# Kernel tuning notes

Measured on AMD Instinct MI355X. Metric: run time of the kernel, lower is better.

Reference implementation:

```python
import jax, jax.numpy as jnp
import numpy as np

HEADS = 16
D_HEAD = 64
EPS = 1e-5


def _ln(x, g, b):
    m = jnp.mean(x, axis=-1, keepdims=True)
    v = jnp.var(x, axis=-1, keepdims=True)
    return (x - m) * jax.lax.rsqrt(v + EPS) * g + b


def _attn(xq, xc, Wq, Wk, Wv, Wo, bo):
    # Wq: [dim, inner], Wk/Wv: [ctx_dim, inner], Wo: [inner, dim]
    B, N, _ = xq.shape
    S = xc.shape[1]
    q = (xq @ Wq).reshape(B, N, HEADS, D_HEAD)
    k = (xc @ Wk).reshape(B, S, HEADS, D_HEAD)
    v = (xc @ Wv).reshape(B, S, HEADS, D_HEAD)
    scale = D_HEAD ** -0.5
    scores = jnp.einsum('bnhd,bshd->bhns', q, k) * scale
    attn = jax.nn.softmax(scores, axis=-1)
    out = jnp.einsum('bhns,bshd->bnhd', attn, v).reshape(B, N, HEADS * D_HEAD)
    return out @ Wo + bo


def _geglu_ff(x, Wp, bp, Wf, bf):
    h = x @ Wp + bp  # [B,N,2*inner]
    a, gate = jnp.split(h, 2, axis=-1)
    # torch F.gelu default is exact (erf) gelu
    return (a * jax.nn.gelu(gate, approximate=False)) @ Wf + bf


def setup_inputs() -> dict:
    key = jax.random.key(0)
    ks = jax.random.split(key, 16)
    dim, ctx, inner, ffin = 1024, 768, HEADS * D_HEAD, 4 * 1024
    def w(k, i, o):
        return jax.random.normal(k, (i, o), jnp.float32) * (i ** -0.5)
    inp = {
        'x': jax.random.normal(ks[0], (4, 2048, dim), jnp.float32),
        'context': jax.random.normal(ks[1], (4, 77, ctx), jnp.float32),
        'Wq1': w(ks[2], dim, inner), 'Wk1': w(ks[3], dim, inner), 'Wv1': w(ks[4], dim, inner),
        'Wo1': w(ks[5], inner, dim), 'bo1': jnp.zeros((dim,), jnp.float32),
        'Wq2': w(ks[6], dim, inner), 'Wk2': w(ks[7], ctx, inner), 'Wv2': w(ks[8], ctx, inner),
        'Wo2': w(ks[9], inner, dim), 'bo2': jnp.zeros((dim,), jnp.float32),
        'Wp': w(ks[10], dim, 2 * ffin), 'bp': jnp.zeros((2 * ffin,), jnp.float32),
        'Wf': w(ks[11], ffin, dim), 'bf': jnp.zeros((dim,), jnp.float32),
        'g1': jnp.ones((dim,), jnp.float32), 'b1': jnp.zeros((dim,), jnp.float32),
        'g2': jnp.ones((dim,), jnp.float32), 'b2': jnp.zeros((dim,), jnp.float32),
        'g3': jnp.ones((dim,), jnp.float32), 'b3': jnp.zeros((dim,), jnp.float32),
    }
    return inp


def reference(x, context, Wq1, Wk1, Wv1, Wo1, bo1, Wq2, Wk2, Wv2, Wo2, bo2,
              Wp, bp, Wf, bf, g1, b1, g2, b2, g3, b3):
    x = _attn(_ln(x, g1, b1), _ln(x, g1, b1), Wq1, Wk1, Wv1, Wo1, bo1) + x
    x = _attn(_ln(x, g2, b2), context, Wq2, Wk2, Wv2, Wo2, bo2) + x
    x = _geglu_ff(_ln(x, g3, b3), Wp, bp, Wf, bf) + x
    return x
```

## Files before the change

### kernel.cpp

```cpp
#include <hip/hip_runtime.h>

typedef unsigned short u16;
typedef __bf16 bf16x8 __attribute__((ext_vector_type(8)));
typedef float f32x4 __attribute__((ext_vector_type(4)));

#define HEADS 16
#define DHEAD 64
#define DIM 1024
#define NTOK 2048
#define BATCH 4
#define CTXD 768
#define SCROSS 77
#define FFIN 4096

__device__ inline float bf2f(u16 v) { return __uint_as_float(((unsigned)v) << 16); }
__device__ inline u16 f2bf(float f) {
    unsigned u = __float_as_uint(f);
    unsigned r = u + 0x7fffu + ((u >> 16) & 1u);
    return (u16)(r >> 16);
}
__device__ inline f32x4 f4zero() { f32x4 v; v[0]=0.f; v[1]=0.f; v[2]=0.f; v[3]=0.f; return v; }
__device__ inline bf16x8 as_bf16x8(uint4 u) { union { uint4 a; bf16x8 b; } c; c.a = u; return c.b; }

__device__ inline void gload_lds16(const u16* g, u16* l) {
    __builtin_amdgcn_global_load_lds((const __attribute__((address_space(1))) unsigned*)g,
                                     (__attribute__((address_space(3))) unsigned*)l, 16, 0, 0);
}

__global__ __launch_bounds__(256) void wt_k(const float* __restrict__ W, u16* __restrict__ WT,
                                            int K, int N, float scale, int remap) {
    __shared__ u16 Ts[64][72];
    int k0 = blockIdx.x * 64, n0 = blockIdx.y * 64;
    int t = threadIdx.x;
    int r = t >> 2, c4 = (t & 3) * 16;
    const float* wp = W + (size_t)(k0 + r) * N + n0 + c4;
    #pragma unroll
    for (int j = 0; j < 4; j++) {
        float4 v = *(const float4*)(wp + j * 4);
        Ts[c4 + j * 4 + 0][r] = f2bf(v.x * scale);
        Ts[c4 + j * 4 + 1][r] = f2bf(v.y * scale);
        Ts[c4 + j * 4 + 2][r] = f2bf(v.z * scale);
        Ts[c4 + j * 4 + 3][r] = f2bf(v.w * scale);
    }
    __syncthreads();
    int n = t >> 2, kc = (t & 3) * 16;
    int ng = n0 + n;
    if (remap) ng = ((ng & 4095) >> 4) * 32 + ((ng >> 12) << 4) + (ng & 15);
    u16* op = WT + (size_t)ng * K + k0 + kc;
    *(uint4*)op       = *(const uint4*)&Ts[n][kc];
    *(uint4*)(op + 8) = *(const uint4*)&Ts[n][kc + 8];
}

__global__ __launch_bounds__(256) void cvt_k(const float* __restrict__ X, u16* __restrict__ Y, int n4) {
    int i = blockIdx.x * 256 + threadIdx.x;
    if (i < n4) {
        float4 v = *(const float4*)(X + (size_t)i * 4);
        uint2 o;
        o.x = (unsigned)f2bf(v.x) | ((unsigned)f2bf(v.y) << 16);
        o.y = (unsigned)f2bf(v.z) | ((unsigned)f2bf(v.w) << 16);
        *(uint2*)(Y + (size_t)i * 4) = o;
    }
}

__global__ __launch_bounds__(256) void ln_k(const float* __restrict__ X, const float* __restrict__ G,
                                            const float* __restrict__ Bt, u16* __restrict__ Y) {
    int row = blockIdx.x;
    int t = threadIdx.x;
    int w = t >> 6, lane = t & 63;
    float4 xv = *(const float4*)(X + (size_t)row * DIM + t * 4);
    float s = xv.x + xv.y + xv.z + xv.w;
    float s2 = xv.x*xv.x + xv.y*xv.y + xv.z*xv.z + xv.w*xv.w;
    for (int off = 1; off < 64; off <<= 1) {
        s  += __shfl_xor(s,  off, 64);
        s2 += __shfl_xor(s2, off, 64);
    }
    __shared__ float rs[4], rs2[4];
    if (lane == 0) { rs[w] = s; rs2[w] = s2; }
    __syncthreads();
    float S_ = rs[0] + rs[1] + rs[2] + rs[3];
    float S2_ = rs2[0] + rs2[1] + rs2[2] + rs2[3];
    float mean = S_ * (1.0f / DIM);
    float var = fmaxf(S2_ * (1.0f / DIM) - mean * mean, 0.f);
    float rstd = rsqrtf(var + 1e-5f);
    int col = t * 4;
    float4 g = *(const float4*)(G + col);
    float4 b = *(const float4*)(Bt + col);
    float y0 = (xv.x - mean) * rstd * g.x + b.x;
    float y1 = (xv.y - mean) * rstd * g.y + b.y;
    float y2 = (xv.z - mean) * rstd * g.z + b.z;
    float y3 = (xv.w - mean) * rstd * g.w + b.w;
    uint2 o;
    o.x = (unsigned)f2bf(y0) | ((unsigned)f2bf(y1) << 16);
    o.y = (unsigned)f2bf(y2) | ((unsigned)f2bf(y3) << 16);
    *(uint2*)(Y + (size_t)row * DIM + col) = o;
}

template<typename TC, bool RESID>
__global__ __launch_bounds__(256) void gemm128(const u16* __restrict__ A, int lda,
                                               const u16* __restrict__ BT,
                                               const float* __restrict__ bias, const float* resid,
                                               TC* C, int ldc, int M, int N, int K) {
    __shared__ __align__(16) u16 As[128 * 32];
    __shared__ __align__(16) u16 Bs[128 * 32];
    int m0 = blockIdx.x * 128, n0 = blockIdx.y * 128;
    int t = threadIdx.x;
    int w = t >> 6, lane = t & 63;
    int quad = lane >> 4, l16 = lane & 15;
    int mh = (w & 1) * 64, nh = (w >> 1) * 64;
    f32x4 acc[4][4];
    #pragma unroll
    for (int i = 0; i < 4; i++)
        #pragma unroll
        for (int j = 0; j < 4; j++) acc[i][j] = f4zero();
    int sr = t >> 2;
    int sc8 = (t & 3) * 8;
    int ra0 = min(m0 + sr, M - 1);
    int ra1 = min(m0 + sr + 64, M - 1);
    const u16* ga0 = A + (size_t)ra0 * lda + sc8;
    const u16* ga1 = A + (size_t)ra1 * lda + sc8;
    const u16* gb0 = BT + (size_t)(n0 + sr) * K + sc8;
    const u16* gb1 = BT + (size_t)(n0 + sr + 64) * K + sc8;
    u16* lA0 = &As[w * 512];
    u16* lA1 = &As[2048 + w * 512];
    u16* lB0 = &Bs[w * 512];
    u16* lB1 = &Bs[2048 + w * 512];
    for (int k0 = 0; k0 < K; k0 += 32) {
        __syncthreads();
        gload_lds16(ga0 + k0, lA0);
        gload_lds16(ga1 + k0, lA1);
        gload_lds16(gb0 + k0, lB0);
        gload_lds16(gb1 + k0, lB1);
        __syncthreads();
        bf16x8 af[4], bfv[4];
        #pragma unroll
        for (int i = 0; i < 4; i++) {
            af[i]  = as_bf16x8(*(const uint4*)&As[(mh + i * 16 + l16) * 32 + quad * 8]);
            bfv[i] = as_bf16x8(*(const uint4*)&Bs[(nh + i * 16 + l16) * 32 + quad * 8]);
        }
        #pragma unroll
        for (int i = 0; i < 4; i++)
            #pragma unroll
            for (int j = 0; j < 4; j++)
                acc[i][j] = __builtin_amdgcn_mfma_f32_16x16x32_bf16(af[i], bfv[j], acc[i][j], 0, 0, 0);
    }
    #pragma unroll
    for (int j = 0; j < 4; j++) {
        int gn = n0 + nh + j * 16 + l16;
        float bv = bias ? bias[gn] : 0.f;
        #pragma unroll
        for (int i = 0; i < 4; i++) {
            #pragma unroll
            for (int r = 0; r < 4; r++) {
                int gm = m0 + mh + i * 16 + quad * 4 + r;
                if (gm < M) {
                    float v = acc[i][j][r] + bv;
                    if constexpr (RESID) v += resid[(size_t)gm * N + gn];
                    if constexpr (__is_same(TC, u16)) C[(size_t)gm * ldc + gn] = f2bf(v);
                    else                              C[(size_t)gm * ldc + gn] = v;
                }
            }
        }
    }
}


#define BAR() __builtin_amdgcn_s_barrier()
#define SB0() __builtin_amdgcn_sched_barrier(0)
#define PRIO1() __builtin_amdgcn_s_setprio(1)
#define PRIO0() __builtin_amdgcn_s_setprio(0)
#define WAIT_VM6() asm volatile("s_waitcnt vmcnt(6)" ::: "memory")
#define WAIT_VM0() asm volatile("s_waitcnt vmcnt(0)" ::: "memory")
#define WAIT_LGKM0() asm volatile("s_waitcnt lgkmcnt(0)" ::: "memory")
#define WAIT_LGKM8() asm volatile("s_waitcnt lgkmcnt(8)" ::: "memory")

#define STAGE_A_R(P, h, q, TAU) gload_lds16(gA + (size_t)((h) * 128 + (q) * 64) * 1024 + (TAU) * 64, \
                                            lA + (P) * 16384 + (h) * 8192 + (q) * 4096)
#define STAGE_B_R(P, h, q, TAU) gload_lds16(gB + (size_t)((h) * 128 + (q) * 64) * 1024 + (TAU) * 64, \
                                            lB + (P) * 16384 + (h) * 8192 + (q) * 4096)
#define RD_A(P, fi, ks) as_bf16x8(*(const uint4*)(rdA + (P) * 32768 + (fi) * 2048 + ((ks) ? o1 : o0)))
#define RD_B(P, fj, ks) as_bf16x8(*(const uint4*)(rdB + (P) * 32768 + (fj) * 2048 + ((ks) ? o1 : o0)))
#define MM(ai, aj, av, bv) acc[ai][aj] = __builtin_amdgcn_mfma_f32_16x16x32_bf16(av, bv, acc[ai][aj], 0, 0, 0)

#define TILE256(P, S0, S1, T, LAST) do {                                              \
    if (LAST) { WAIT_VM0(); } else { WAIT_VM6(); }                                    \
    BAR(); SB0();                                                                     \
                               \
    Ar[0][0] = RD_A(P, 0, 0); Ar[0][1] = RD_A(P, 0, 1);                               \
    Ar[1][0] = RD_A(P, 1, 0); Ar[1][1] = RD_A(P, 1, 1);                               \
    Ar[2][0] = RD_A(P, 2, 0); Ar[2][1] = RD_A(P, 2, 1);                               \
    Ar[3][0] = RD_A(P, 3, 0); Ar[3][1] = RD_A(P, 3, 1);                               \
    Br[0][0] = RD_B(P, 0, 0); Br[0][1] = RD_B(P, 0, 1);                               \
    Br[1][0] = RD_B(P, 1, 0); Br[1][1] = RD_B(P, 1, 1);                               \
    if (S0) { STAGE_B_R((P) ^ 1, 1, 0, (T) + 1); STAGE_B_R((P) ^ 1, 1, 1, (T) + 1); } \
    WAIT_LGKM8();                                                                     \
    BAR(); WAIT_LGKM0(); SB0(); PRIO1();                                              \
    MM(0,0,Ar[0][0],Br[0][0]); MM(1,0,Ar[1][0],Br[0][0]); MM(2,0,Ar[2][0],Br[0][0]); MM(3,0,Ar[3][0],Br[0][0]); \
    MM(0,1,Ar[0][0],Br[1][0]); MM(1,1,Ar[1][0],Br[1][0]); MM(2,1,Ar[2][0],Br[1][0]); MM(3,1,Ar[3][0],Br[1][0]); \
    MM(0,0,Ar[0][1],Br[0][1]); MM(1,0,Ar[1][1],Br[0][1]); MM(2,0,Ar[2][1],Br[0][1]); MM(3,0,Ar[3][1],Br[0][1]); \
    MM(0,1,Ar[0][1],Br[1][1]); MM(1,1,Ar[1][1],Br[1][1]); MM(2,1,Ar[2][1],Br[1][1]); MM(3,1,Ar[3][1],Br[1][1]); \
    PRIO0(); SB0(); BAR();                                                            \
                                                   \
    Br[0][0] = RD_B(P, 2, 0); Br[0][1] = RD_B(P, 2, 1);                               \
    Br[1][0] = RD_B(P, 3, 0); Br[1][1] = RD_B(P, 3, 1);                               \
    if (S1) { STAGE_A_R(P, 0, 0, (T) + 2); STAGE_A_R(P, 1, 0, (T) + 2); }             \
    BAR(); WAIT_LGKM0(); SB0(); PRIO1();                                              \
    MM(0,2,Ar[0][0],Br[0][0]); MM(1,2,Ar[1][0],Br[0][0]); MM(2,2,Ar[2][0],Br[0][0]); MM(3,2,Ar[3][0],Br[0][0]); \
    MM(0,3,Ar[0][0],Br[1][0]); MM(1,3,Ar[1][0],Br[1][0]); MM(2,3,Ar[2][0],Br[1][0]); MM(3,3,Ar[3][0],Br[1][0]); \
    MM(0,2,Ar[0][1],Br[0][1]); MM(1,2,Ar[1][1],Br[0][1]); MM(2,2,Ar[2][1],Br[0][1]); MM(3,2,Ar[3][1],Br[0][1]); \
    MM(0,3,Ar[0][1],Br[1][1]); MM(1,3,Ar[1][1],Br[1][1]); MM(2,3,Ar[2][1],Br[1][1]); MM(3,3,Ar[3][1],Br[1][1]); \
    PRIO0(); SB0(); BAR();                                                            \
                                                  \
    Ar[0][0] = RD_A(P, 4, 0); Ar[0][1] = RD_A(P, 4, 1);                               \
    Ar[1][0] = RD_A(P, 5, 0); Ar[1][1] = RD_A(P, 5, 1);                               \
    Ar[2][0] = RD_A(P, 6, 0); Ar[2][1] = RD_A(P, 6, 1);                               \
    Ar[3][0] = RD_A(P, 7, 0); Ar[3][1] = RD_A(P, 7, 1);                               \
    if (S1) { STAGE_A_R(P, 0, 1, (T) + 2); STAGE_A_R(P, 1, 1, (T) + 2); }             \
    BAR(); WAIT_LGKM0(); SB0(); PRIO1();                                              \
    MM(4,2,Ar[0][0],Br[0][0]); MM(5,2,Ar[1][0],Br[0][0]); MM(6,2,Ar[2][0],Br[0][0]); MM(7,2,Ar[3][0],Br[0][0]); \
    MM(4,3,Ar[0][0],Br[1][0]); MM(5,3,Ar[1][0],Br[1][0]); MM(6,3,Ar[2][0],Br[1][0]); MM(7,3,Ar[3][0],Br[1][0]); \
    MM(4,2,Ar[0][1],Br[0][1]); MM(5,2,Ar[1][1],Br[0][1]); MM(6,2,Ar[2][1],Br[0][1]); MM(7,2,Ar[3][1],Br[0][1]); \
    MM(4,3,Ar[0][1],Br[1][1]); MM(5,3,Ar[1][1],Br[1][1]); MM(6,3,Ar[2][1],Br[1][1]); MM(7,3,Ar[3][1],Br[1][1]); \
    PRIO0(); SB0(); BAR();                                                            \
                                              \
    Br[0][0] = RD_B(P, 0, 0); Br[0][1] = RD_B(P, 0, 1);                               \
    Br[1][0] = RD_B(P, 1, 0); Br[1][1] = RD_B(P, 1, 1);                               \
    if (S1) { STAGE_B_R(P, 0, 0, (T) + 2); STAGE_B_R(P, 0, 1, (T) + 2); }             \
    BAR(); WAIT_LGKM0(); SB0(); PRIO1();                                              \
    MM(4,0,Ar[0][0],Br[0][0]); MM(5,0,Ar[1][0],Br[0][0]); MM(6,0,Ar[2][0],Br[0][0]); MM(7,0,Ar[3][0],Br[0][0]); \
    MM(4,1,Ar[0][0],Br[1][0]); MM(5,1,Ar[1][0],Br[1][0]); MM(6,1,Ar[2][0],Br[1][0]); MM(7,1,Ar[3][0],Br[1][0]); \
    MM(4,0,Ar[0][1],Br[0][1]); MM(5,0,Ar[1][1],Br[0][1]); MM(6,0,Ar[2][1],Br[0][1]); MM(7,0,Ar[3][1],Br[0][1]); \
    MM(4,1,Ar[0][1],Br[1][1]); MM(5,1,Ar[1][1],Br[1][1]); MM(6,1,Ar[2][1],Br[1][1]); MM(7,1,Ar[3][1],Br[1][1]); \
    PRIO0(); SB0();                                                                   \
} while (0)

template<int NBY, int LDC, int EPI>
__global__ __launch_bounds__(512, 2) void gemm256(const u16* __restrict__ A,
                                                  const u16* __restrict__ BT,
                                                  const float* __restrict__ bias,
                                                  u16* __restrict__ C) {
    __shared__ __align__(16) u16 As[2][16384];
    __shared__ __align__(16) u16 Bs[2][16384];
    int t = threadIdx.x;
    int w = t >> 6, lane = t & 63;
    int quad = lane >> 4, l16 = lane & 15;
    int wm = w >> 2, wn = w & 3;
    int bid = blockIdx.x;
    int cpx = (int)gridDim.x >> 3;
    int swz = (bid & 7) * cpx + (bid >> 3);
    int bx = swz / NBY, by = swz % NBY;
    int m0 = bx << 8, n0 = by << 8;

    int ar = t >> 3;
    int ac = (((t & 7) ^ (ar & 7)) << 3);
    const u16* gA = A + (size_t)(m0 + ar) * 1024 + ac;
    const u16* gB = BT + (size_t)(n0 + ar) * 1024 + ac;
    u16* lA = &As[0][0] + (w << 9);
    u16* lB = &Bs[0][0] + (w << 9);
    const char* rdA = (const char*)&As[0][0] + (((wm << 7) + l16) << 7);
    const char* rdB = (const char*)&Bs[0][0] + (((wn << 6) + l16) << 7);
    int o0 = (quad << 4) ^ ((l16 & 7) << 4);
    int o1 = o0 ^ 64;

    f32x4 acc[8][4];
    #pragma unroll
    for (int i = 0; i < 8; i++)
        #pragma unroll
        for (int j = 0; j < 4; j++) acc[i][j] = f4zero();

    STAGE_A_R(0, 0, 0, 0); STAGE_A_R(0, 0, 1, 0); STAGE_A_R(0, 1, 0, 0); STAGE_A_R(0, 1, 1, 0);
    STAGE_B_R(0, 0, 0, 0); STAGE_B_R(0, 0, 1, 0); STAGE_B_R(0, 1, 0, 0); STAGE_B_R(0, 1, 1, 0);
    STAGE_A_R(1, 0, 0, 1); STAGE_A_R(1, 0, 1, 1); STAGE_A_R(1, 1, 0, 1); STAGE_A_R(1, 1, 1, 1);
    STAGE_B_R(1, 0, 0, 1); STAGE_B_R(1, 0, 1, 1);

    bf16x8 Ar[4][2], Br[2][2];
    #pragma unroll 1
    for (int tt = 0; tt < 14; tt += 2) {
        TILE256(0, 1, 1, tt, 0);
        TILE256(1, 1, 1, tt + 1, 0);
    }
    TILE256(0, 1, 0, 14, 0);
    TILE256(1, 0, 0, 15, 1);

    if constexpr (EPI == 0) {
        int gm0 = m0 + wm * 128 + quad * 4;
        int gn0 = n0 + wn * 64 + l16;
        #pragma unroll
        for (int fi = 0; fi < 8; fi++)
            #pragma unroll
            for (int fj = 0; fj < 4; fj++)
                #pragma unroll
                for (int r = 0; r < 4; r++)
                    C[(size_t)(gm0 + fi * 16 + r) * LDC + gn0 + fj * 16] = f2bf(acc[fi][fj][r]);
    } else {
        int gm0 = m0 + wm * 128 + quad * 4;
        int oc0 = (n0 >> 1) + wn * 32 + l16;
        #pragma unroll
        for (int jp = 0; jp < 2; jp++) {
            int oc = oc0 + jp * 16;
            float ba = bias[oc];
            float bg = bias[FFIN + oc];
            #pragma unroll
            for (int fi = 0; fi < 8; fi++)
                #pragma unroll
                for (int r = 0; r < 4; r++) {
                    float a = acc[fi][2 * jp][r] + ba;
                    float g = acc[fi][2 * jp + 1][r] + bg;
                    float v = a * (0.5f * g * (1.f + erff(g * 0.70710678118654752f)));
                    C[(size_t)(gm0 + fi * 16 + r) * LDC + oc] = f2bf(v);
                }
        }
    }
}

__global__ __launch_bounds__(256) void attn_k(const u16* Q, int ldq, const u16* __restrict__ K,
                                              const u16* __restrict__ V, int ldkv,
                                              u16* O, int S) {
    __shared__ __align__(16) u16 Ksh[2][4096];
    __shared__ __align__(16) u16 Vt[4][2048];
    __shared__ __align__(16) u16 Pb[4][4][512];
    int bh = blockIdx.x;
    int b = bh >> 4, h = bh & 15;
    int q0 = blockIdx.y * 64;
    int t = threadIdx.x;
    int w = t >> 6, lane = t & 63;
    int quad = lane >> 4, l16 = lane & 15;
    const u16* Qp = Q + ((size_t)b * NTOK + q0) * ldq + h * DHEAD;
    const u16* Kp = K + (size_t)b * S * ldkv + h * DHEAD;
    const u16* Vp = V + (size_t)b * S * ldkv + h * DHEAD;
    bf16x8 qf[2];
    #pragma unroll
    for (int ds = 0; ds < 2; ds++)
        qf[ds] = as_bf16x8(*(const uint4*)(Qp + (size_t)(w * 16 + l16) * ldq + ds * 32 + quad * 8));
    float l_l = 0.f;
    f32x4 o_acc[4];
    #pragma unroll
    for (int dt = 0; dt < 4; dt++) o_acc[dt] = f4zero();
    int cA = w * 128 + lane;
    int krA = cA >> 2, kdA = (cA & 3) * 8;
    int krB = (cA + 64) >> 2, kdB = ((cA + 64) & 3) * 8;
    int vd = (t >> 5) * 8;
    int vk = (t & 31) * 4;
    int vkk = vk >> 5, vcol = vk & 31;
    int nkt = (S + 127) / 128;
    for (int kt = 0; kt < nkt; kt++) {
        int kbase = kt * 128;
        bool full = (kbase + 128) <= S;
        __syncthreads();
        {
            int rA = min(kbase + krA, S - 1);
            int rB = min(kbase + krB, S - 1);
            const u16* kgA = Kp + (size_t)rA * ldkv;
            const u16* kgB = Kp + (size_t)rB * ldkv;
            gload_lds16(kgA + kdA,      &Ksh[0][w * 1024]);
            gload_lds16(kgB + kdB,      &Ksh[0][w * 1024 + 512]);
            gload_lds16(kgA + 32 + kdA, &Ksh[1][w * 1024]);
            gload_lds16(kgB + 32 + kdB, &Ksh[1][w * 1024 + 512]);
        }
        {
            union { uint4 u; u16 e[8]; } vr[4];
            #pragma unroll
            for (int j = 0; j < 4; j++) {
                int key = min(kbase + vk + j, S - 1);
                vr[j].u = *(const uint4*)(Vp + (size_t)key * ldkv + vd);
            }
            #pragma unroll
            for (int d = 0; d < 8; d++) {
                uint2 p;
                p.x = (unsigned)vr[0].e[d] | ((unsigned)vr[1].e[d] << 16);
                p.y = (unsigned)vr[2].e[d] | ((unsigned)vr[3].e[d] << 16);
                *(uint2*)&Vt[vkk][(vd + d) * 32 + vcol] = p;
            }
        }
        __syncthreads();
        f32x4 sc[8];
        #pragma unroll
        for (int sub = 0; sub < 8; sub++) {
            bf16x8 kf0 = as_bf16x8(*(const uint4*)&Ksh[0][(sub * 16 + l16) * 32 + quad * 8]);
            bf16x8 kf1 = as_bf16x8(*(const uint4*)&Ksh[1][(sub * 16 + l16) * 32 + quad * 8]);
            f32x4 s = __builtin_amdgcn_mfma_f32_16x16x32_bf16(kf0, qf[0], f4zero(), 0, 0, 0);
            sc[sub] = __builtin_amdgcn_mfma_f32_16x16x32_bf16(kf1, qf[1], s, 0, 0, 0);
        }
        if (!full) {
            #pragma unroll
            for (int sub = 0; sub < 8; sub++)
                #pragma unroll
                for (int r = 0; r < 4; r++)
                    if (kbase + sub * 16 + quad * 4 + r >= S) sc[sub][r] = -1e30f;
        }
        float psum = 0.f;
        #pragma unroll
        for (int sub = 0; sub < 8; sub++) {
            float p0 = __builtin_amdgcn_exp2f(sc[sub][0]);
            float p1 = __builtin_amdgcn_exp2f(sc[sub][1]);
            float p2 = __builtin_amdgcn_exp2f(sc[sub][2]);
            float p3 = __builtin_amdgcn_exp2f(sc[sub][3]);
            psum += (p0 + p1) + (p2 + p3);
            uint2 pk;
            pk.x = __builtin_amdgcn_perm(__float_as_uint(p1), __float_as_uint(p0), 0x07060302);
            pk.y = __builtin_amdgcn_perm(__float_as_uint(p3), __float_as_uint(p2), 0x07060302);
            *(uint2*)&Pb[w][sub >> 1][l16 * 32 + (sub & 1) * 16 + quad * 4] = pk;
        }
        l_l += psum;
        #pragma unroll
        for (int kk = 0; kk < 4; kk++) {
            bf16x8 pf = as_bf16x8(*(const uint4*)&Pb[w][kk][l16 * 32 + quad * 8]);
            #pragma unroll
            for (int dt = 0; dt < 4; dt++) {
                bf16x8 vf = as_bf16x8(*(const uint4*)&Vt[kk][(dt * 16 + l16) * 32 + quad * 8]);
                o_acc[dt] = __builtin_amdgcn_mfma_f32_16x16x32_bf16(pf, vf, o_acc[dt], 0, 0, 0);
            }
        }
    }
    float l_tot = l_l;
    l_tot += __shfl_xor(l_tot, 16, 64);
    l_tot += __shfl_xor(l_tot, 32, 64);
    #pragma unroll
    for (int r = 0; r < 4; r++) {
        float lr = __shfl(l_tot, quad * 4 + r, 64);
        float invl = (lr > 0.f) ? (1.f / lr) : 0.f;
        int gq = q0 + w * 16 + quad * 4 + r;
        #pragma unroll
        for (int dt = 0; dt < 4; dt++) {
            O[((size_t)b * NTOK + gq) * ldq + h * DHEAD + dt * 16 + l16] = f2bf(o_acc[dt][r] * invl);
        }
    }
}

extern "C" void kernel_launch(void* const* d_in, const int* in_sizes, int n_in,
                              void* d_out, int out_size, void* d_ws, size_t ws_size,
                              hipStream_t stream) {
    const float* x   = (const float*)d_in[0];
    const float* ctx = (const float*)d_in[1];
    const float* Wq1 = (const float*)d_in[2];
    const float* Wk1 = (const float*)d_in[3];
    const float* Wv1 = (const float*)d_in[4];
    const float* Wo1 = (const float*)d_in[5];
    const float* bo1 = (const float*)d_in[6];
    const float* Wq2 = (const float*)d_in[7];
    const float* Wk2 = (const float*)d_in[8];
    const float* Wv2 = (const float*)d_in[9];
    const float* Wo2 = (const float*)d_in[10];
    const float* bo2 = (const float*)d_in[11];
    const float* Wp  = (const float*)d_in[12];
    const float* bp  = (const float*)d_in[13];
    const float* Wf  = (const float*)d_in[14];
    const float* bfb = (const float*)d_in[15];
    const float* g1  = (const float*)d_in[16];
    const float* b1  = (const float*)d_in[17];
    const float* g2  = (const float*)d_in[18];
    const float* b2  = (const float*)d_in[19];
    const float* g3  = (const float*)d_in[20];
    const float* b3  = (const float*)d_in[21];
    float* out = (float*)d_out;

    const int M = BATCH * NTOK;
    const int Mc = BATCH * SCROSS;
    u16* ws = (u16*)d_ws;
    size_t o = 0;
    u16* WqT1 = ws + o; o += (size_t)DIM * DIM;
    u16* WkT1 = ws + o; o += (size_t)DIM * DIM;
    u16* WvT1 = ws + o; o += (size_t)DIM * DIM;
    u16* WoT1 = ws + o; o += (size_t)DIM * DIM;
    u16* WqT2 = ws + o; o += (size_t)DIM * DIM;
    u16* WoT2 = ws + o; o += (size_t)DIM * DIM;
    u16* WkT2 = ws + o; o += (size_t)DIM * CTXD;
    u16* WvT2 = ws + o; o += (size_t)DIM * CTXD;
    u16* WpT  = ws + o; o += (size_t)(2 * FFIN) * DIM;
    u16* WfT  = ws + o; o += (size_t)DIM * FFIN;
    u16* ctxb = ws + o; o += (size_t)Mc * CTXD;
    u16* KVc  = ws + o; o += (size_t)Mc * 2048;
    u16* P    = ws + o; o += (size_t)M * DIM;
    u16* QKV  = ws + o; o += (size_t)M * 3072;
    u16* reg2 = ws + o; o += (size_t)M * DIM * 2;
    float* X1 = (float*)reg2;
    u16* gb = QKV;

    dim3 blk(256);
    const float qscale = 0.125f * 1.4426950408889634f;

    wt_k<<<dim3(16, 16), blk, 0, stream>>>(Wq1, WqT1, DIM, DIM, qscale, 0);
    wt_k<<<dim3(16, 16), blk, 0, stream>>>(Wk1, WkT1, DIM, DIM, 1.f, 0);
    wt_k<<<dim3(16, 16), blk, 0, stream>>>(Wv1, WvT1, DIM, DIM, 1.f, 0);
    wt_k<<<dim3(16, 16), blk, 0, stream>>>(Wo1, WoT1, DIM, DIM, 1.f, 0);
    wt_k<<<dim3(16, 16), blk, 0, stream>>>(Wq2, WqT2, DIM, DIM, qscale, 0);
    wt_k<<<dim3(16, 16), blk, 0, stream>>>(Wo2, WoT2, DIM, DIM, 1.f, 0);
    wt_k<<<dim3(12, 16), blk, 0, stream>>>(Wk2, WkT2, CTXD, DIM, 1.f, 0);
    wt_k<<<dim3(12, 16), blk, 0, stream>>>(Wv2, WvT2, CTXD, DIM, 1.f, 0);
    wt_k<<<dim3(16, 128), blk, 0, stream>>>(Wp, WpT, DIM, 2 * FFIN, 1.f, 1);
    wt_k<<<dim3(64, 16), blk, 0, stream>>>(Wf, WfT, FFIN, DIM, 1.f, 0);
    cvt_k<<<dim3((Mc * CTXD / 4 + 255) / 256), blk, 0, stream>>>(ctx, ctxb, Mc * CTXD / 4);

    ln_k<<<dim3(M), blk, 0, stream>>>(x, g1, b1, P);
    gemm256<12, 3072, 0><<<dim3(32 * 12), dim3(512), 0, stream>>>(P, WqT1, nullptr, QKV);
    attn_k<<<dim3(BATCH * HEADS, NTOK / 64), blk, 0, stream>>>(
        QKV, 3072, QKV + 1024, QKV + 2048, 3072, QKV, NTOK);
    gemm128<float, true><<<dim3(M / 128, DIM / 128), blk, 0, stream>>>(
        QKV, 3072, WoT1, bo1, x, X1, DIM, M, DIM, DIM);

    ln_k<<<dim3(M), blk, 0, stream>>>(X1, g2, b2, P);
    gemm128<u16, false><<<dim3(M / 128, DIM / 128), blk, 0, stream>>>(
        P, DIM, WqT2, nullptr, nullptr, QKV, 3072, M, DIM, DIM);
    gemm128<u16, false><<<dim3((Mc + 127) / 128, 2048 / 128), blk, 0, stream>>>(
        ctxb, CTXD, WkT2, nullptr, nullptr, KVc, 2048, Mc, 2048, CTXD);
    attn_k<<<dim3(BATCH * HEADS, NTOK / 64), blk, 0, stream>>>(
        QKV, 3072, KVc, KVc + 1024, 2048, QKV, SCROSS);
    gemm128<float, true><<<dim3(M / 128, DIM / 128), blk, 0, stream>>>(
        QKV, 3072, WoT2, bo2, X1, out, DIM, M, DIM, DIM);

    ln_k<<<dim3(M), blk, 0, stream>>>(out, g3, b3, P);
    gemm256<32, 4096, 1><<<dim3(32 * 32), dim3(512), 0, stream>>>(P, WpT, bp, gb);
    gemm128<float, true><<<dim3(M / 128, DIM / 128), blk, 0, stream>>>(
        gb, FFIN, WfT, bfb, out, out, DIM, M, DIM, FFIN);
}
```

Before: 949.6 us.

## Swizzle LDS layouts in GEMM and attention, reorder gemm256 pipeline, use gemm128 for QKV

Adds XOR swizzling to the LDS tiles of gemm128 and attn_k to cut bank conflicts, and widens the attention K/V/P tiles to one 128-wide layout. gemm256 now holds two B register sets so it can reorder its MFMA phases and drop one LDS read and one wait, and its prologue staging order changes. The QKV projection moves from gemm256 to gemm128, and attention raises wave priority around its MFMA blocks. These are several separate changes bundled together; the QKV switch may lose the deeper pipelining of gemm256.

New measurement: 912.9 us. -3.9%, faster.

```diff
diff --git a/kernel.cpp b/kernel.cpp
--- a/kernel.cpp
+++ b/kernel.cpp
@@ -113,7 +113,7 @@
         #pragma unroll
         for (int j = 0; j < 4; j++) acc[i][j] = f4zero();
     int sr = t >> 2;
-    int sc8 = (t & 3) * 8;
+    int sc8 = (((t & 3) ^ ((sr >> 1) & 3)) * 8);
     int ra0 = min(m0 + sr, M - 1);
     int ra1 = min(m0 + sr + 64, M - 1);
     const u16* ga0 = A + (size_t)ra0 * lda + sc8;
@@ -124,6 +124,7 @@
     u16* lA1 = &As[2048 + w * 512];
     u16* lB0 = &Bs[w * 512];
     u16* lB1 = &Bs[2048 + w * 512];
+    int rq = ((quad ^ ((l16 >> 1) & 3)) * 8);
     for (int k0 = 0; k0 < K; k0 += 32) {
         __syncthreads();
         gload_lds16(ga0 + k0, lA0);
@@ -134,8 +135,8 @@
         bf16x8 af[4], bfv[4];
         #pragma unroll
         for (int i = 0; i < 4; i++) {
-            af[i]  = as_bf16x8(*(const uint4*)&As[(mh + i * 16 + l16) * 32 + quad * 8]);
-            bfv[i] = as_bf16x8(*(const uint4*)&Bs[(nh + i * 16 + l16) * 32 + quad * 8]);
+            af[i]  = as_bf16x8(*(const uint4*)&As[(mh + i * 16 + l16) * 32 + rq]);
+            bfv[i] = as_bf16x8(*(const uint4*)&Bs[(nh + i * 16 + l16) * 32 + rq]);
         }
         #pragma unroll
         for (int i = 0; i < 4; i++)
@@ -184,52 +185,50 @@
 #define TILE256(P, S0, S1, T, LAST) do {                                              \
     if (LAST) { WAIT_VM0(); } else { WAIT_VM6(); }                                    \
     BAR(); SB0();                                                                     \
-                               \
+                        \
     Ar[0][0] = RD_A(P, 0, 0); Ar[0][1] = RD_A(P, 0, 1);                               \
     Ar[1][0] = RD_A(P, 1, 0); Ar[1][1] = RD_A(P, 1, 1);                               \
     Ar[2][0] = RD_A(P, 2, 0); Ar[2][1] = RD_A(P, 2, 1);                               \
     Ar[3][0] = RD_A(P, 3, 0); Ar[3][1] = RD_A(P, 3, 1);                               \
-    Br[0][0] = RD_B(P, 0, 0); Br[0][1] = RD_B(P, 0, 1);                               \
-    Br[1][0] = RD_B(P, 1, 0); Br[1][1] = RD_B(P, 1, 1);                               \
+    BrA[0][0] = RD_B(P, 0, 0); BrA[0][1] = RD_B(P, 0, 1);                             \
+    BrA[1][0] = RD_B(P, 1, 0); BrA[1][1] = RD_B(P, 1, 1);                             \
     if (S0) { STAGE_B_R((P) ^ 1, 1, 0, (T) + 1); STAGE_B_R((P) ^ 1, 1, 1, (T) + 1); } \
     WAIT_LGKM8();                                                                     \
     BAR(); WAIT_LGKM0(); SB0(); PRIO1();                                              \
-    MM(0,0,Ar[0][0],Br[0][0]); MM(1,0,Ar[1][0],Br[0][0]); MM(2,0,Ar[2][0],Br[0][0]); MM(3,0,Ar[3][0],Br[0][0]); \
-    MM(0,1,Ar[0][0],Br[1][0]); MM(1,1,Ar[1][0],Br[1][0]); MM(2,1,Ar[2][0],Br[1][0]); MM(3,1,Ar[3][0],Br[1][0]); \
-    MM(0,0,Ar[0][1],Br[0][1]); MM(1,0,Ar[1][1],Br[0][1]); MM(2,0,Ar[2][1],Br[0][1]); MM(3,0,Ar[3][1],Br[0][1]); \
-    MM(0,1,Ar[0][1],Br[1][1]); MM(1,1,Ar[1][1],Br[1][1]); MM(2,1,Ar[2][1],Br[1][1]); MM(3,1,Ar[3][1],Br[1][1]); \
+    MM(0,0,Ar[0][0],BrA[0][0]); MM(1,0,Ar[1][0],BrA[0][0]); MM(2,0,Ar[2][0],BrA[0][0]); MM(3,0,Ar[3][0],BrA[0][0]); \
+    MM(0,1,Ar[0][0],BrA[1][0]); MM(1,1,Ar[1][0],BrA[1][0]); MM(2,1,Ar[2][0],BrA[1][0]); MM(3,1,Ar[3][0],BrA[1][0]); \
+    MM(0,0,Ar[0][1],BrA[0][1]); MM(1,0,Ar[1][1],BrA[0][1]); MM(2,0,Ar[2][1],BrA[0][1]); MM(3,0,Ar[3][1],BrA[0][1]); \
+    MM(0,1,Ar[0][1],BrA[1][1]); MM(1,1,Ar[1][1],BrA[1][1]); MM(2,1,Ar[2][1],BrA[1][1]); MM(3,1,Ar[3][1],BrA[1][1]); \
     PRIO0(); SB0(); BAR();                                                            \
-                                                   \
-    Br[0][0] = RD_B(P, 2, 0); Br[0][1] = RD_B(P, 2, 1);                               \
-    Br[1][0] = RD_B(P, 3, 0); Br[1][1] = RD_B(P, 3, 1);                               \
+                                       \
+    BrB[0][0] = RD_B(P, 2, 0); BrB[0][1] = RD_B(P, 2, 1);                             \
+    BrB[1][0] = RD_B(P, 3, 0); BrB[1][1] = RD_B(P, 3, 1);                             \
     if (S1) { STAGE_A_R(P, 0, 0, (T) + 2); STAGE_A_R(P, 1, 0, (T) + 2); }             \
     BAR(); WAIT_LGKM0(); SB0(); PRIO1();                                              \
-    MM(0,2,Ar[0][0],Br[0][0]); MM(1,2,Ar[1][0],Br[0][0]); MM(2,2,Ar[2][0],Br[0][0]); MM(3,2,Ar[3][0],Br[0][0]); \
-    MM(0,3,Ar[0][0],Br[1][0]); MM(1,3,Ar[1][0],Br[1][0]); MM(2,3,Ar[2][0],Br[1][0]); MM(3,3,Ar[3][0],Br[1][0]); \
-    MM(0,2,Ar[0][1],Br[0][1]); MM(1,2,Ar[1][1],Br[0][1]); MM(2,2,Ar[2][1],Br[0][1]); MM(3,2,Ar[3][1],Br[0][1]); \
-    MM(0,3,Ar[0][1],Br[1][1]); MM(1,3,Ar[1][1],Br[1][1]); MM(2,3,Ar[2][1],Br[1][1]); MM(3,3,Ar[3][1],Br[1][1]); \
+    MM(0,2,Ar[0][0],BrB[0][0]); MM(1,2,Ar[1][0],BrB[0][0]); MM(2,2,Ar[2][0],BrB[0][0]); MM(3,2,Ar[3][0],BrB[0][0]); \
+    MM(0,3,Ar[0][0],BrB[1][0]); MM(1,3,Ar[1][0],BrB[1][0]); MM(2,3,Ar[2][0],BrB[1][0]); MM(3,3,Ar[3][0],BrB[1][0]); \
+    MM(0,2,Ar[0][1],BrB[0][1]); MM(1,2,Ar[1][1],BrB[0][1]); MM(2,2,Ar[2][1],BrB[0][1]); MM(3,2,Ar[3][1],BrB[0][1]); \
+    MM(0,3,Ar[0][1],BrB[1][1]); MM(1,3,Ar[1][1],BrB[1][1]); MM(2,3,Ar[2][1],BrB[1][1]); MM(3,3,Ar[3][1],BrB[1][1]); \
     PRIO0(); SB0(); BAR();                                                            \
-                                                  \
+      \
     Ar[0][0] = RD_A(P, 4, 0); Ar[0][1] = RD_A(P, 4, 1);                               \
     Ar[1][0] = RD_A(P, 5, 0); Ar[1][1] = RD_A(P, 5, 1);                               \
     Ar[2][0] = RD_A(P, 6, 0); Ar[2][1] = RD_A(P, 6, 1);                               \
     Ar[3][0] = RD_A(P, 7, 0); Ar[3][1] = RD_A(P, 7, 1);                               \
-    if (S1) { STAGE_A_R(P, 0, 1, (T) + 2); STAGE_A_R(P, 1, 1, (T) + 2); }             \
-    BAR(); WAIT_LGKM0(); SB0(); PRIO1();                                              \
-    MM(4,2,Ar[0][0],Br[0][0]); MM(5,2,Ar[1][0],Br[0][0]); MM(6,2,Ar[2][0],Br[0][0]); MM(7,2,Ar[3][0],Br[0][0]); \
-    MM(4,3,Ar[0][0],Br[1][0]); MM(5,3,Ar[1][0],Br[1][0]); MM(6,3,Ar[2][0],Br[1][0]); MM(7,3,Ar[3][0],Br[1][0]); \
-    MM(4,2,Ar[0][1],Br[0][1]); MM(5,2,Ar[1][1],Br[0][1]); MM(6,2,Ar[2][1],Br[0][1]); MM(7,2,Ar[3][1],Br[0][1]); \
-    MM(4,3,Ar[0][1],Br[1][1]); MM(5,3,Ar[1][1],Br[1][1]); MM(6,3,Ar[2][1],Br[1][1]); MM(7,3,Ar[3][1],Br[1][1]); \
-    PRIO0(); SB0(); BAR();                                                            \
-                                              \
-    Br[0][0] = RD_B(P, 0, 0); Br[0][1] = RD_B(P, 0, 1);                               \
-    Br[1][0] = RD_B(P, 1, 0); Br[1][1] = RD_B(P, 1, 1);                               \
     if (S1) { STAGE_B_R(P, 0, 0, (T) + 2); STAGE_B_R(P, 0, 1, (T) + 2); }             \
     BAR(); WAIT_LGKM0(); SB0(); PRIO1();                                              \
-    MM(4,0,Ar[0][0],Br[0][0]); MM(5,0,Ar[1][0],Br[0][0]); MM(6,0,Ar[2][0],Br[0][0]); MM(7,0,Ar[3][0],Br[0][0]); \
-    MM(4,1,Ar[0][0],Br[1][0]); MM(5,1,Ar[1][0],Br[1][0]); MM(6,1,Ar[2][0],Br[1][0]); MM(7,1,Ar[3][0],Br[1][0]); \
-    MM(4,0,Ar[0][1],Br[0][1]); MM(5,0,Ar[1][1],Br[0][1]); MM(6,0,Ar[2][1],Br[0][1]); MM(7,0,Ar[3][1],Br[0][1]); \
-    MM(4,1,Ar[0][1],Br[1][1]); MM(5,1,Ar[1][1],Br[1][1]); MM(6,1,Ar[2][1],Br[1][1]); MM(7,1,Ar[3][1],Br[1][1]); \
+    MM(4,2,Ar[0][0],BrB[0][0]); MM(5,2,Ar[1][0],BrB[0][0]); MM(6,2,Ar[2][0],BrB[0][0]); MM(7,2,Ar[3][0],BrB[0][0]); \
+    MM(4,3,Ar[0][0],BrB[1][0]); MM(5,3,Ar[1][0],BrB[1][0]); MM(6,3,Ar[2][0],BrB[1][0]); MM(7,3,Ar[3][0],BrB[1][0]); \
+    MM(4,2,Ar[0][1],BrB[0][1]); MM(5,2,Ar[1][1],BrB[0][1]); MM(6,2,Ar[2][1],BrB[0][1]); MM(7,2,Ar[3][1],BrB[0][1]); \
+    MM(4,3,Ar[0][1],BrB[1][1]); MM(5,3,Ar[1][1],BrB[1][1]); MM(6,3,Ar[2][1],BrB[1][1]); MM(7,3,Ar[3][1],BrB[1][1]); \
+    PRIO0(); SB0(); BAR();                                                            \
+           \
+    if (S1) { STAGE_A_R(P, 0, 1, (T) + 2); STAGE_A_R(P, 1, 1, (T) + 2); }             \
+    BAR(); SB0(); PRIO1();                                                            \
+    MM(4,0,Ar[0][0],BrA[0][0]); MM(5,0,Ar[1][0],BrA[0][0]); MM(6,0,Ar[2][0],BrA[0][0]); MM(7,0,Ar[3][0],BrA[0][0]); \
+    MM(4,1,Ar[0][0],BrA[1][0]); MM(5,1,Ar[1][0],BrA[1][0]); MM(6,1,Ar[2][0],BrA[1][0]); MM(7,1,Ar[3][0],BrA[1][0]); \
+    MM(4,0,Ar[0][1],BrA[0][1]); MM(5,0,Ar[1][1],BrA[0][1]); MM(6,0,Ar[2][1],BrA[0][1]); MM(7,0,Ar[3][1],BrA[0][1]); \
+    MM(4,1,Ar[0][1],BrA[1][1]); MM(5,1,Ar[1][1],BrA[1][1]); MM(6,1,Ar[2][1],BrA[1][1]); MM(7,1,Ar[3][1],BrA[1][1]); \
     PRIO0(); SB0();                                                                   \
 } while (0)
 
@@ -267,12 +266,15 @@
         #pragma unroll
         for (int j = 0; j < 4; j++) acc[i][j] = f4zero();
 
-    STAGE_A_R(0, 0, 0, 0); STAGE_A_R(0, 0, 1, 0); STAGE_A_R(0, 1, 0, 0); STAGE_A_R(0, 1, 1, 0);
-    STAGE_B_R(0, 0, 0, 0); STAGE_B_R(0, 0, 1, 0); STAGE_B_R(0, 1, 0, 0); STAGE_B_R(0, 1, 1, 0);
-    STAGE_A_R(1, 0, 0, 1); STAGE_A_R(1, 0, 1, 1); STAGE_A_R(1, 1, 0, 1); STAGE_A_R(1, 1, 1, 1);
+    STAGE_A_R(0, 0, 0, 0); STAGE_A_R(0, 1, 0, 0);
+    STAGE_B_R(0, 0, 0, 0); STAGE_B_R(0, 0, 1, 0);
+    STAGE_A_R(0, 0, 1, 0); STAGE_A_R(0, 1, 1, 0);
+    STAGE_B_R(0, 1, 0, 0); STAGE_B_R(0, 1, 1, 0);
+    STAGE_A_R(1, 0, 0, 1); STAGE_A_R(1, 1, 0, 1);
     STAGE_B_R(1, 0, 0, 1); STAGE_B_R(1, 0, 1, 1);
-
-    bf16x8 Ar[4][2], Br[2][2];
+    STAGE_A_R(1, 0, 1, 1); STAGE_A_R(1, 1, 1, 1);
+
+    bf16x8 Ar[4][2], BrA[2][2], BrB[2][2];
     #pragma unroll 1
     for (int tt = 0; tt < 14; tt += 2) {
         TILE256(0, 1, 1, tt, 0);
@@ -315,15 +317,16 @@
 __global__ __launch_bounds__(256) void attn_k(const u16* Q, int ldq, const u16* __restrict__ K,
                                               const u16* __restrict__ V, int ldkv,
                                               u16* O, int S) {
-    __shared__ __align__(16) u16 Ksh[2][4096];
-    __shared__ __align__(16) u16 Vt[4][2048];
-    __shared__ __align__(16) u16 Pb[4][4][512];
+    __shared__ __align__(16) u16 Ksh[128 * 64];
+    __shared__ __align__(16) u16 Vt[64 * 128];
+    __shared__ __align__(16) u16 Pb[4][16 * 128];
     int bh = blockIdx.x;
     int b = bh >> 4, h = bh & 15;
     int q0 = blockIdx.y * 64;
     int t = threadIdx.x;
     int w = t >> 6, lane = t & 63;
     int quad = lane >> 4, l16 = lane & 15;
+    int sw = (l16 & 7) << 3;
     const u16* Qp = Q + ((size_t)b * NTOK + q0) * ldq + h * DHEAD;
     const u16* Kp = K + (size_t)b * S * ldkv + h * DHEAD;
     const u16* Vp = V + (size_t)b * S * ldkv + h * DHEAD;
@@ -335,26 +338,19 @@
     f32x4 o_acc[4];
     #pragma unroll
     for (int dt = 0; dt < 4; dt++) o_acc[dt] = f4zero();
-    int cA = w * 128 + lane;
-    int krA = cA >> 2, kdA = (cA & 3) * 8;
-    int krB = (cA + 64) >> 2, kdB = ((cA + 64) & 3) * 8;
+    int kr8 = lane >> 3;
+    int ksl = ((lane & 7) ^ kr8) * 8;
     int vd = (t >> 5) * 8;
     int vk = (t & 31) * 4;
-    int vkk = vk >> 5, vcol = vk & 31;
     int nkt = (S + 127) / 128;
     for (int kt = 0; kt < nkt; kt++) {
         int kbase = kt * 128;
         bool full = (kbase + 128) <= S;
         __syncthreads();
-        {
-            int rA = min(kbase + krA, S - 1);
-            int rB = min(kbase + krB, S - 1);
-            const u16* kgA = Kp + (size_t)rA * ldkv;
-            const u16* kgB = Kp + (size_t)rB * ldkv;
-            gload_lds16(kgA + kdA,      &Ksh[0][w * 1024]);
-            gload_lds16(kgB + kdB,      &Ksh[0][w * 1024 + 512]);
-            gload_lds16(kgA + 32 + kdA, &Ksh[1][w * 1024]);
-            gload_lds16(kgB + 32 + kdB, &Ksh[1][w * 1024 + 512]);
+        #pragma unroll
+        for (int i = 0; i < 4; i++) {
+            int r = min(kbase + (i * 4 + w) * 8 + kr8, S - 1);
+            gload_lds16(Kp + (size_t)r * ldkv + ksl, &Ksh[(i * 4 + w) * 512]);
         }
         {
             union { uint4 u; u16 e[8]; } vr[4];
@@ -365,21 +361,25 @@
             }
             #pragma unroll
             for (int d = 0; d < 8; d++) {
+                int row = vd + d;
                 uint2 p;
                 p.x = (unsigned)vr[0].e[d] | ((unsigned)vr[1].e[d] << 16);
                 p.y = (unsigned)vr[2].e[d] | ((unsigned)vr[3].e[d] << 16);
-                *(uint2*)&Vt[vkk][(vd + d) * 32 + vcol] = p;
+                *(uint2*)&Vt[row * 128 + (vk ^ ((row & 7) << 3))] = p;
             }
         }
         __syncthreads();
         f32x4 sc[8];
+        PRIO1();
         #pragma unroll
         for (int sub = 0; sub < 8; sub++) {
-            bf16x8 kf0 = as_bf16x8(*(const uint4*)&Ksh[0][(sub * 16 + l16) * 32 + quad * 8]);
-            bf16x8 kf1 = as_bf16x8(*(const uint4*)&Ksh[1][(sub * 16 + l16) * 32 + quad * 8]);
+            const u16* kr = &Ksh[(sub * 16 + l16) * 64];
+            bf16x8 kf0 = as_bf16x8(*(const uint4*)(kr + ((quad * 8) ^ sw)));
+            bf16x8 kf1 = as_bf16x8(*(const uint4*)(kr + ((32 + quad * 8) ^ sw)));
             f32x4 s = __builtin_amdgcn_mfma_f32_16x16x32_bf16(kf0, qf[0], f4zero(), 0, 0, 0);
             sc[sub] = __builtin_amdgcn_mfma_f32_16x16x32_bf16(kf1, qf[1], s, 0, 0, 0);
         }
+        PRIO0();
         if (!full) {
             #pragma unroll
             for (int sub = 0; sub < 8; sub++)
@@ -398,18 +398,20 @@
             uint2 pk;
             pk.x = __builtin_amdgcn_perm(__float_as_uint(p1), __float_as_uint(p0), 0x07060302);
             pk.y = __builtin_amdgcn_perm(__float_as_uint(p3), __float_as_uint(p2), 0x07060302);
-            *(uint2*)&Pb[w][sub >> 1][l16 * 32 + (sub & 1) * 16 + quad * 4] = pk;
+            *(uint2*)&Pb[w][l16 * 128 + ((sub * 16 + quad * 4) ^ sw)] = pk;
         }
         l_l += psum;
+        PRIO1();
         #pragma unroll
         for (int kk = 0; kk < 4; kk++) {
-            bf16x8 pf = as_bf16x8(*(const uint4*)&Pb[w][kk][l16 * 32 + quad * 8]);
+            bf16x8 pf = as_bf16x8(*(const uint4*)&Pb[w][l16 * 128 + ((kk * 32 + quad * 8) ^ sw)]);
             #pragma unroll
             for (int dt = 0; dt < 4; dt++) {
-                bf16x8 vf = as_bf16x8(*(const uint4*)&Vt[kk][(dt * 16 + l16) * 32 + quad * 8]);
+                bf16x8 vf = as_bf16x8(*(const uint4*)&Vt[(dt * 16 + l16) * 128 + ((kk * 32 + quad * 8) ^ sw)]);
                 o_acc[dt] = __builtin_amdgcn_mfma_f32_16x16x32_bf16(pf, vf, o_acc[dt], 0, 0, 0);
             }
         }
+        PRIO0();
     }
     float l_tot = l_l;
     l_tot += __shfl_xor(l_tot, 16, 64);
@@ -491,7 +493,8 @@
     cvt_k<<<dim3((Mc * CTXD / 4 + 255) / 256), blk, 0, stream>>>(ctx, ctxb, Mc * CTXD / 4);
 
     ln_k<<<dim3(M), blk, 0, stream>>>(x, g1, b1, P);
-    gemm256<12, 3072, 0><<<dim3(32 * 12), dim3(512), 0, stream>>>(P, WqT1, nullptr, QKV);
+    gemm128<u16, false><<<dim3(M / 128, 3072 / 128), blk, 0, stream>>>(
+        P, DIM, WqT1, nullptr, nullptr, QKV, 3072, M, 3072, DIM);
     attn_k<<<dim3(BATCH * HEADS, NTOK / 64), blk, 0, stream>>>(
         QKV, 3072, QKV + 1024, QKV + 2048, 3072, QKV, NTOK);
     gemm128<float, true><<<dim3(M / 128, DIM / 128), blk, 0, stream>>>(
```
